# Kernel tuning notes

Hardware: AMD Instinct MI355X
Metric: run time of the kernel (lower is better)

The kernel has to match this reference:

```python
import jax, jax.numpy as jnp
import numpy as np

N, E = 100000, 3200000
F_IN, HID, NCLS = 1433, 8, 7
H1, H2 = 8, 1
NEG_SLOPE = 0.2


def gat_layer(x, W, att_src, att_dst, bias, src, dst, heads, ch):
    n = x.shape[0]
    h = (x @ W).reshape(n, heads, ch)                      # [N,H,C]
    a_s = (h * att_src).sum(-1)                            # [N,H]
    a_d = (h * att_dst).sum(-1)                            # [N,H]
    e = a_s[src] + a_d[dst]                                # [Etot,H]
    e = jnp.where(e > 0, e, NEG_SLOPE * e)                 # leaky_relu(0.2)
    m = jax.ops.segment_max(e, dst, num_segments=n)        # per-dst max
    e = jnp.exp(e - m[dst])
    denom = jax.ops.segment_sum(e, dst, num_segments=n)
    alpha = e / (denom[dst] + 1e-16)                       # segment softmax
    msg = h[src] * alpha[:, :, None]                       # [Etot,H,C]
    out = jax.ops.segment_sum(msg, dst, num_segments=n)    # [N,H,C]
    return out.mean(axis=1) + bias                         # concat=False -> head mean


def setup_inputs() -> dict:
    key = jax.random.key(0)
    ks = jax.random.split(key, 10)
    x = jax.random.normal(ks[0], (N, F_IN), dtype=jnp.float32)
    edge_index = jax.random.randint(ks[1], (2, E), 0, N, dtype=jnp.int32)
    s = 0.1
    W1 = jax.random.normal(ks[2], (F_IN, H1 * HID), dtype=jnp.float32) * s
    att_src1 = jax.random.normal(ks[3], (H1, HID), dtype=jnp.float32) * s
    att_dst1 = jax.random.normal(ks[4], (H1, HID), dtype=jnp.float32) * s
    b1 = jnp.zeros((HID,), dtype=jnp.float32)
    W2 = jax.random.normal(ks[5], (HID, H2 * NCLS), dtype=jnp.float32) * s
    att_src2 = jax.random.normal(ks[6], (H2, NCLS), dtype=jnp.float32) * s
    att_dst2 = jax.random.normal(ks[7], (H2, NCLS), dtype=jnp.float32) * s
    b2 = jnp.zeros((NCLS,), dtype=jnp.float32)
    return {"x": x, "edge_index": edge_index, "W1": W1, "att_src1": att_src1,
            "att_dst1": att_dst1, "b1": b1, "W2": W2, "att_src2": att_src2,
            "att_dst2": att_dst2, "b2": b2}


def reference(x, edge_index, W1, att_src1, att_dst1, b1, W2, att_src2, att_dst2, b2):
    n = x.shape[0]
    loops = jnp.arange(n, dtype=edge_index.dtype)
    src = jnp.concatenate([edge_index[0], loops])  # PyG add_self_loops=True
    dst = jnp.concatenate([edge_index[1], loops])
    h = jax.nn.elu(gat_layer(x, W1, att_src1, att_dst1, b1, src, dst, H1, HID))
    out = gat_layer(h, W2, att_src2, att_dst2, b2, src, dst, H2, NCLS)
    return jax.nn.log_softmax(out, axis=-1)
```

## Files before the change

### kernel.cpp

```cpp
#include <hip/hip_runtime.h>

#define N_NODES 100000
#define E_EDGES 3200000
#define F_IN    1433
#define K_PAD   1472
#define NCH     98
#define KPH     64

typedef _Float16 f16x4 __attribute__((ext_vector_type(4)));
typedef _Float16 f16x8 __attribute__((ext_vector_type(8)));
typedef float    f32x4 __attribute__((ext_vector_type(4)));

__device__ __forceinline__ void gload_lds16(const void* g, void* l) {
    __builtin_amdgcn_global_load_lds(
        (const __attribute__((address_space(1))) unsigned int*)g,
        (__attribute__((address_space(3))) unsigned int*)l, 16, 0, 0);
}

__global__ void k_init(const float* __restrict__ w1, _Float16* __restrict__ w1t,
                       int* __restrict__ counts) {
    int i = blockIdx.x * 256 + threadIdx.x;
    if (i < N_NODES) counts[i] = 0;
    if (i < 64 * K_PAD) {
        int n = i / K_PAD, k = i - n * K_PAD;
        float v = (k < F_IN) ? w1[(size_t)k * 64 + n] : 0.f;
        w1t[i] = (_Float16)v;
    }
}

__global__ void k_hist(const int* __restrict__ dst, int* __restrict__ counts) {
    int idx = blockIdx.x * 256 + threadIdx.x;
    int4 d4 = ((const int4*)dst)[idx];
    atomicAdd(&counts[d4.x], 1);
    atomicAdd(&counts[d4.y], 1);
    atomicAdd(&counts[d4.z], 1);
    atomicAdd(&counts[d4.w], 1);
}

__global__ void k_scan_a(const int* __restrict__ counts, int* __restrict__ csum) {
    __shared__ int sh[256];
    int b = blockIdx.x, t = threadIdx.x;
    int s = 0;
    for (int j = 0; j < 4; ++j) {
        int idx = b * 1024 + j * 256 + t;
        if (idx < N_NODES) s += counts[idx];
    }
    sh[t] = s; __syncthreads();
    for (int off = 128; off > 0; off >>= 1) {
        if (t < off) sh[t] += sh[t + off];
        __syncthreads();
    }
    if (t == 0) csum[b] = sh[0];
}

__global__ void k_scan_b(int* __restrict__ csum) {
    __shared__ int sh[128];
    int t = threadIdx.x;
    int v = (t < NCH) ? csum[t] : 0;
    sh[t] = v; __syncthreads();
    for (int off = 1; off < 128; off <<= 1) {
        int u = (t >= off) ? sh[t - off] : 0;
        __syncthreads();
        sh[t] += u;
        __syncthreads();
    }
    if (t < NCH) csum[t] = sh[t] - v;
}

__global__ void k_scan_c(const int* __restrict__ counts, const int* __restrict__ csum,
                         int* __restrict__ offsets, int* __restrict__ cursor) {
    __shared__ int sh[256];
    int b = blockIdx.x, t = threadIdx.x;
    int base = b * 1024 + t * 4;
    int c0 = (base + 0 < N_NODES) ? counts[base + 0] : 0;
    int c1 = (base + 1 < N_NODES) ? counts[base + 1] : 0;
    int c2 = (base + 2 < N_NODES) ? counts[base + 2] : 0;
    int c3 = (base + 3 < N_NODES) ? counts[base + 3] : 0;
    int tot = c0 + c1 + c2 + c3;
    sh[t] = tot; __syncthreads();
    for (int off = 1; off < 256; off <<= 1) {
        int v = (t >= off) ? sh[t - off] : 0;
        __syncthreads();
        sh[t] += v;
        __syncthreads();
    }
    int excl = sh[t] - tot;
    int o = csum[b] + excl;
    if (base + 0 < N_NODES) { offsets[base + 0] = o;            cursor[base + 0] = o; }
    if (base + 1 < N_NODES) { int q = o + c0;      offsets[base + 1] = q; cursor[base + 1] = q; }
    if (base + 2 < N_NODES) { int q = o + c0 + c1; offsets[base + 2] = q; cursor[base + 2] = q; }
    if (base + 3 < N_NODES) { int q = o + c0 + c1 + c2; offsets[base + 3] = q; cursor[base + 3] = q; }
}

__global__ __launch_bounds__(256) void k_gemm_scat(const float* __restrict__ x,
                                                   const _Float16* __restrict__ w1t,
                                                   const float* __restrict__ att_src1,
                                                   const float* __restrict__ att_dst1,
                                                   _Float16* __restrict__ h1,
                                                   float* __restrict__ a_s1,
                                                   float* __restrict__ a_d1,
                                                   const int* __restrict__ src,
                                                   const int* __restrict__ dst,
                                                   int* __restrict__ cursor,
                                                   int* __restrict__ sorted_src) {
    __shared__ __align__(16) char AsB[2][64 * 256];
    __shared__ __align__(16) char BsB[2][64 * 128];
    const int tid = threadIdx.x;

    if (blockIdx.x & 1) {
        const int sid = blockIdx.x >> 1;
        for (int sweep = 0; sweep < 7; ++sweep) {
            #pragma unroll
            for (int rep = 0; rep < 2; ++rep) {
                int i4 = sid * 512 + rep * 256 + tid;
                if (i4 < E_EDGES / 4) {
                    int4 s4 = ((const int4*)src)[i4];
                    int4 d4 = ((const int4*)dst)[i4];
                    int p;
                    if ((d4.x >> 14) == sweep) { p = atomicAdd(&cursor[d4.x], 1); sorted_src[p] = s4.x; }
                    if ((d4.y >> 14) == sweep) { p = atomicAdd(&cursor[d4.y], 1); sorted_src[p] = s4.y; }
                    if ((d4.z >> 14) == sweep) { p = atomicAdd(&cursor[d4.z], 1); sorted_src[p] = s4.z; }
                    if ((d4.w >> 14) == sweep) { p = atomicAdd(&cursor[d4.w], 1); sorted_src[p] = s4.w; }
                }
            }
        }
        return;
    }

    const int gid  = blockIdx.x >> 1;
    const int lane = tid & 63;
    const int wave = tid >> 6;
    const int l16  = lane & 15;
    const int l4   = lane >> 4;
    const int brow0 = gid * 64;

    f32x4 acc[4] = {};

    auto stageA = [&](int buf, int ph) {
        #pragma unroll
        for (int j = 0; j < 4; ++j) {
            int p = j * 256 + tid;
            int row = p >> 4, q = p & 15;
            int qs = q ^ (row & 7);
            int grow = brow0 + row; if (grow > N_NODES - 1) grow = N_NODES - 1;
            const float* gp = x + (size_t)grow * F_IN + ph * KPH + qs * 4;
            gload_lds16(gp, AsB[buf] + j * 4096 + wave * 1024);
        }
    };
    auto stageB = [&](int buf, int ph) {
        #pragma unroll
        for (int j = 0; j < 2; ++j) {
            int p = j * 256 + tid;
            int col = p >> 3, c = p & 7;
            int cs = c ^ (col & 7);
            const _Float16* gp = w1t + (size_t)col * K_PAD + ph * KPH + cs * 8;
            gload_lds16(gp, BsB[buf] + j * 4096 + wave * 1024);
        }
    };
    auto stageTailA = [&](int buf) {
        for (int i = tid; i < 1024; i += 256) {
            int row = i >> 4, q = i & 15;
            int qs = q ^ (row & 7);
            int grow = brow0 + row; if (grow > N_NODES - 1) grow = N_NODES - 1;
            const float* gp = x + (size_t)grow * F_IN;
            float4 v;
            #pragma unroll
            for (int jj = 0; jj < 4; ++jj) {
                int k = 1408 + qs * 4 + jj;
                ((float*)&v)[jj] = (k < F_IN) ? gp[k] : 0.f;
            }
            *(float4*)(AsB[buf] + row * 256 + q * 16) = v;
        }
    };
    auto compute = [&](int buf) {
        const int rA = wave * 16 + l16;
        const char* Ab = AsB[buf] + rA * 256;
        const int r7 = rA & 7;
        #pragma unroll
        for (int st = 0; st < 4; ++st) {
            float4 af = *(const float4*)(Ab + ((((st << 2) + l4) ^ r7) << 4));
            f16x4 a = { (_Float16)af.x, (_Float16)af.y, (_Float16)af.z, (_Float16)af.w };
            #pragma unroll
            for (int t = 0; t < 4; ++t) {
                const int cB = t * 16 + l16;
                const int chunk = (st << 1) + (l4 >> 1);
                const int boff = cB * 128 + ((chunk ^ (cB & 7)) << 4) + ((l4 & 1) << 3);
                f16x4 b = *(const f16x4*)(BsB[buf] + boff);
                acc[t] = __builtin_amdgcn_mfma_f32_16x16x16f16(a, b, acc[t], 0, 0, 0);
            }
        }
    };

    stageA(0, 0); stageB(0, 0);
    stageA(1, 1); stageB(1, 1);
    for (int ph = 0; ph <= 20; ++ph) {
        asm volatile("s_waitcnt vmcnt(6)" ::: "memory");
        __builtin_amdgcn_sched_barrier(0);
        __builtin_amdgcn_s_barrier();
        compute(ph & 1);
        asm volatile("s_waitcnt lgkmcnt(0)" ::: "memory");
        __builtin_amdgcn_s_barrier();
        int nxt = ph + 2;
        if (nxt < 22)       { stageA(ph & 1, nxt); stageB(ph & 1, nxt); }
        else if (nxt == 22) { stageTailA(ph & 1);  stageB(ph & 1, 22);  }
    }
    asm volatile("s_waitcnt vmcnt(0) lgkmcnt(0)" ::: "memory");
    __builtin_amdgcn_sched_barrier(0);
    __builtin_amdgcn_s_barrier();
    compute(1);
    compute(0);

    const int wrow0 = brow0 + wave * 16;
    #pragma unroll
    for (int t = 0; t < 4; ++t) {
        const int head = t * 2 + (l16 >> 3);
        const int ch   = l16 & 7;
        const float asc = att_src1[head * 8 + ch];
        const float adc = att_dst1[head * 8 + ch];
        #pragma unroll
        for (int j = 0; j < 4; ++j) {
            int r = wrow0 + l4 * 4 + j;
            float ps = acc[t][j] * asc, pd = acc[t][j] * adc;
            ps += __shfl_xor(ps, 1); ps += __shfl_xor(ps, 2); ps += __shfl_xor(ps, 4);
            pd += __shfl_xor(pd, 1); pd += __shfl_xor(pd, 2); pd += __shfl_xor(pd, 4);
            if (r < N_NODES) {
                h1[(size_t)r * 64 + t * 16 + l16] = (_Float16)acc[t][j];
                if (ch == 0) {
                    a_s1[r * 8 + head] = ps;
                    a_d1[r * 8 + head] = pd;
                }
            }
        }
    }
}

__global__ __launch_bounds__(256) void k_agg1(
    const int* __restrict__ offsets, const int* __restrict__ counts,
    const int* __restrict__ sorted_src,
    const float* __restrict__ a_s1, const float* __restrict__ a_d1,
    const _Float16* __restrict__ h1, const float* __restrict__ b1,
    const float* __restrict__ w2, const float* __restrict__ att_src2,
    const float* __restrict__ att_dst2,
    _Float16* __restrict__ g, float* __restrict__ a_s2, float* __restrict__ a_d2) {
    const int lane = threadIdx.x & 63;
    const int wave = threadIdx.x >> 6;
    const int h    = lane & 7;
    const int es   = lane >> 3;
    const int n    = blockIdx.x * 4 + wave;
    const int start = offsets[n];
    const int cnt   = counts[n];
    const float adn = a_d1[n * 8 + h];
    float et = a_s1[n * 8 + h] + adn;
    const float e_self = et > 0.f ? et : 0.2f * et;

    float m = e_self, denom = 0.f;
    float acc[8] = {0.f,0.f,0.f,0.f,0.f,0.f,0.f,0.f};
    if (es == 0) {
        denom = 1.f;
        f16x8 hv0 = *(const f16x8*)(h1 + (size_t)n * 64 + h * 8);
        #pragma unroll
        for (int c = 0; c < 8; ++c) acc[c] = (float)hv0[c];
    }
    for (int i = es; i < cnt; i += 64) {
        int   sx[8];
        float ax[8];
        f16x8 vx[8];
        bool  bx[8];
        #pragma unroll
        for (int u = 0; u < 8; ++u) {
            int iu = i + u * 8;
            bx[u] = iu < cnt;
            sx[u] = sorted_src[start + (bx[u] ? iu : i)];
        }
        #pragma unroll
        for (int u = 0; u < 8; ++u) ax[u] = a_s1[sx[u] * 8 + h];
        #pragma unroll
        for (int u = 0; u < 8; ++u) vx[u] = *(const f16x8*)(h1 + (size_t)sx[u] * 64 + h * 8);
        #pragma unroll
        for (int u = 0; u < 8; ++u) {
            if (bx[u]) {
                float e = ax[u] + adn; e = e > 0.f ? e : 0.2f * e;
                if (e > m + 8.f) {
                    float sc = __expf(m - e); denom *= sc;
                    #pragma unroll
                    for (int c = 0; c < 8; ++c) acc[c] *= sc;
                    m = e;
                }
                float p = __expf(e - m); denom += p;
                #pragma unroll
                for (int c = 0; c < 8; ++c) acc[c] += p * (float)vx[u][c];
            }
        }
    }
    #pragma unroll
    for (int d = 8; d < 64; d <<= 1) {
        float mo = __shfl_xor(m, d);
        float dn = __shfl_xor(denom, d);
        float mn = fmaxf(m, mo);
        float sa = __expf(m - mn), sb = __expf(mo - mn);
        denom = denom * sa + dn * sb;
        #pragma unroll
        for (int c = 0; c < 8; ++c) {
            float ao = __shfl_xor(acc[c], d);
            acc[c] = acc[c] * sa + ao * sb;
        }
        m = mn;
    }
    float inv = 1.f / (denom + 1e-16f);
    float hc[8];
    #pragma unroll
    for (int c = 0; c < 8; ++c) {
        float v = acc[c] * inv;
        v += __shfl_xor(v, 1);
        v += __shfl_xor(v, 2);
        v += __shfl_xor(v, 4);
        float o = 0.125f * v + b1[c];
        hc[c] = o > 0.f ? o : expm1f(o);
    }
    if (lane == 0) {
        float s2 = 0.f, d2 = 0.f;
        f16x8 gr;
        #pragma unroll
        for (int j = 0; j < 7; ++j) {
            float t = 0.f;
            #pragma unroll
            for (int c = 0; c < 8; ++c) t += hc[c] * w2[c * 7 + j];
            gr[j] = (_Float16)t;
            s2 += t * att_src2[j];
            d2 += t * att_dst2[j];
        }
        gr[7] = (_Float16)0.f;
        *(f16x8*)(g + (size_t)n * 8) = gr;
        a_s2[n] = s2;
        a_d2[n] = d2;
    }
}

__global__ __launch_bounds__(256) void k_agg2(
    const int* __restrict__ offsets, const int* __restrict__ counts,
    const int* __restrict__ sorted_src,
    const float* __restrict__ a_s2, const float* __restrict__ a_d2,
    const _Float16* __restrict__ g, const float* __restrict__ b2,
    float* __restrict__ outp) {
    const int tid  = threadIdx.x;
    const int lane = tid & 63;
    const int wave = tid >> 6;
    const int grp  = lane >> 3;
    const int s    = lane & 7;
    const int n    = blockIdx.x * 32 + wave * 8 + grp;
    const int start = offsets[n];
    const int cnt   = counts[n];
    const float adn = a_d2[n];
    float et = a_s2[n] + adn;
    const float e_self = et > 0.f ? et : 0.2f * et;

    float m = e_self, denom = 0.f;
    float acc[8] = {0.f,0.f,0.f,0.f,0.f,0.f,0.f,0.f};
    if (s == 0) {
        denom = 1.f;
        f16x8 gv0 = *(const f16x8*)(g + (size_t)n * 8);
        #pragma unroll
        for (int c = 0; c < 8; ++c) acc[c] = (float)gv0[c];
    }
    for (int i = s; i < cnt; i += 64) {
        int   sx[8];
        float ax[8];
        f16x8 vx[8];
        bool  bx[8];
        #pragma unroll
        for (int u = 0; u < 8; ++u) {
            int iu = i + u * 8;
            bx[u] = iu < cnt;
            sx[u] = sorted_src[start + (bx[u] ? iu : i)];
        }
        #pragma unroll
        for (int u = 0; u < 8; ++u) ax[u] = a_s2[sx[u]];
        #pragma unroll
        for (int u = 0; u < 8; ++u) vx[u] = *(const f16x8*)(g + (size_t)sx[u] * 8);
        #pragma unroll
        for (int u = 0; u < 8; ++u) {
            if (bx[u]) {
                float e = ax[u] + adn; e = e > 0.f ? e : 0.2f * e;
                if (e > m + 8.f) {
                    float sc = __expf(m - e); denom *= sc;
                    #pragma unroll
                    for (int c = 0; c < 8; ++c) acc[c] *= sc;
                    m = e;
                }
                float p = __expf(e - m); denom += p;
                #pragma unroll
                for (int c = 0; c < 8; ++c) acc[c] += p * (float)vx[u][c];
            }
        }
    }
    #pragma unroll
    for (int d = 1; d < 8; d <<= 1) {
        float mo = __shfl_xor(m, d, 8);
        float dn = __shfl_xor(denom, d, 8);
        float mn = fmaxf(m, mo);
        float sa = __expf(m - mn), sb = __expf(mo - mn);
        denom = denom * sa + dn * sb;
        #pragma unroll
        for (int c = 0; c < 8; ++c) {
            float ao = __shfl_xor(acc[c], d, 8);
            acc[c] = acc[c] * sa + ao * sb;
        }
        m = mn;
    }
    float inv = 1.f / (denom + 1e-16f);
    float o[7]; float mx = -1e30f;
    #pragma unroll
    for (int c = 0; c < 7; ++c) { o[c] = acc[c] * inv + b2[c]; mx = fmaxf(mx, o[c]); }
    float se = 0.f;
    #pragma unroll
    for (int c = 0; c < 7; ++c) se += __expf(o[c] - mx);
    float ls = mx + logf(se);
    if (s < 7) outp[n * 7 + s] = o[s] - ls;
}

extern "C" void kernel_launch(void* const* d_in, const int* in_sizes, int n_in,
                              void* d_out, int out_size, void* d_ws, size_t ws_size,
                              hipStream_t stream) {
    const float* x        = (const float*)d_in[0];
    const int*   ei       = (const int*)d_in[1];
    const float* W1       = (const float*)d_in[2];
    const float* att_src1 = (const float*)d_in[3];
    const float* att_dst1 = (const float*)d_in[4];
    const float* b1       = (const float*)d_in[5];
    const float* W2       = (const float*)d_in[6];
    const float* att_src2 = (const float*)d_in[7];
    const float* att_dst2 = (const float*)d_in[8];
    const float* b2       = (const float*)d_in[9];
    const int* src = ei;
    const int* dst = ei + E_EDGES;

    char* ws = (char*)d_ws;
    size_t off = 0;
    auto alloc = [&](size_t bytes) -> char* {
        char* p = ws + off;
        off = (off + bytes + 255) & ~(size_t)255;
        return p;
    };
    _Float16* h1         = (_Float16*)alloc((size_t)N_NODES * 64 * 2);
    float*    a_s1       = (float*)   alloc((size_t)N_NODES * 8 * 4);
    float*    a_d1       = (float*)   alloc((size_t)N_NODES * 8 * 4);
    _Float16* w1t        = (_Float16*)alloc((size_t)64 * K_PAD * 2);
    int*      counts     = (int*)     alloc((size_t)N_NODES * 4);
    int*      offsets    = (int*)     alloc((size_t)N_NODES * 4);
    int*      cursor     = (int*)     alloc((size_t)N_NODES * 4);
    int*      csum       = (int*)     alloc((size_t)NCH * 4);
    int*      sorted_src = (int*)     alloc((size_t)(E_EDGES + 32) * 4);
    _Float16* gbuf       = (_Float16*)alloc((size_t)N_NODES * 8 * 2);
    float*    a_s2       = (float*)   alloc((size_t)N_NODES * 4);
    float*    a_d2       = (float*)   alloc((size_t)N_NODES * 4);
    float*    outp       = (float*)d_out;

    hipLaunchKernelGGL(k_init,      dim3(391),   dim3(256), 0, stream, W1, w1t, counts);
    hipLaunchKernelGGL(k_hist,      dim3(3125),  dim3(256), 0, stream, dst, counts);
    hipLaunchKernelGGL(k_scan_a,    dim3(NCH),   dim3(256), 0, stream, counts, csum);
    hipLaunchKernelGGL(k_scan_b,    dim3(1),     dim3(128), 0, stream, csum);
    hipLaunchKernelGGL(k_scan_c,    dim3(NCH),   dim3(256), 0, stream, counts, csum, offsets, cursor);
    hipLaunchKernelGGL(k_gemm_scat, dim3(3126),  dim3(256), 0, stream,
                       x, w1t, att_src1, att_dst1, h1, a_s1, a_d1,
                       src, dst, cursor, sorted_src);
    hipLaunchKernelGGL(k_agg1,      dim3(25000), dim3(256), 0, stream, offsets, counts, sorted_src,
                       a_s1, a_d1, h1, b1, W2, att_src2, att_dst2, gbuf, a_s2, a_d2);
    hipLaunchKernelGGL(k_agg2,      dim3(3125),  dim3(256), 0, stream, offsets, counts, sorted_src,
                       a_s2, a_d2, gbuf, b2, outp);
}
```

Measured before the change: 538.6 us.

## Split scatter from GEMM and use single-wave 32-row GEMM blocks without barriers

The edge scatter, previously interleaved with GEMM blocks in one kernel, becomes its own kernel. The first-layer GEMM is rewritten as 64-thread single-wavefront blocks, each covering 32 rows with two row tiles, so the workgroup s_barriers disappear and each block reuses its B tile across more rows. Tail handling is restructured and the row clamp is dropped because 100000 divides evenly by 32. This gives up concurrent overlap of the atomic scatter with the GEMM and adds a kernel launch. In return it aims for less sync and better per-wave B reuse.

```diff
diff --git a/kernel.cpp b/kernel.cpp
--- a/kernel.cpp
+++ b/kernel.cpp
@@ -92,77 +92,70 @@
     if (base + 3 < N_NODES) { int q = o + c0 + c1 + c2; offsets[base + 3] = q; cursor[base + 3] = q; }
 }
 
-__global__ __launch_bounds__(256) void k_gemm_scat(const float* __restrict__ x,
-                                                   const _Float16* __restrict__ w1t,
-                                                   const float* __restrict__ att_src1,
-                                                   const float* __restrict__ att_dst1,
-                                                   _Float16* __restrict__ h1,
-                                                   float* __restrict__ a_s1,
-                                                   float* __restrict__ a_d1,
-                                                   const int* __restrict__ src,
-                                                   const int* __restrict__ dst,
-                                                   int* __restrict__ cursor,
-                                                   int* __restrict__ sorted_src) {
-    __shared__ __align__(16) char AsB[2][64 * 256];
+__global__ void k_scatter(const int* __restrict__ src, const int* __restrict__ dst,
+                          int* __restrict__ cursor, int* __restrict__ sorted_src) {
+    const int tid = threadIdx.x;
+    const int sid = blockIdx.x;
+    for (int sweep = 0; sweep < 7; ++sweep) {
+        #pragma unroll
+        for (int rep = 0; rep < 2; ++rep) {
+            int i4 = sid * 512 + rep * 256 + tid;
+            if (i4 < E_EDGES / 4) {
+                int4 s4 = ((const int4*)src)[i4];
+                int4 d4 = ((const int4*)dst)[i4];
+                int p;
+                if ((d4.x >> 14) == sweep) { p = atomicAdd(&cursor[d4.x], 1); sorted_src[p] = s4.x; }
+                if ((d4.y >> 14) == sweep) { p = atomicAdd(&cursor[d4.y], 1); sorted_src[p] = s4.y; }
+                if ((d4.z >> 14) == sweep) { p = atomicAdd(&cursor[d4.z], 1); sorted_src[p] = s4.z; }
+                if ((d4.w >> 14) == sweep) { p = atomicAdd(&cursor[d4.w], 1); sorted_src[p] = s4.w; }
+            }
+        }
+    }
+}
+
+__global__ __launch_bounds__(64) void k_gemm1(const float* __restrict__ x,
+                                              const _Float16* __restrict__ w1t,
+                                              const float* __restrict__ att_src1,
+                                              const float* __restrict__ att_dst1,
+                                              _Float16* __restrict__ h1,
+                                              float* __restrict__ a_s1,
+                                              float* __restrict__ a_d1) {
+    __shared__ __align__(16) char AsB[2][32 * 256];
     __shared__ __align__(16) char BsB[2][64 * 128];
-    const int tid = threadIdx.x;
-
-    if (blockIdx.x & 1) {
-        const int sid = blockIdx.x >> 1;
-        for (int sweep = 0; sweep < 7; ++sweep) {
-            #pragma unroll
-            for (int rep = 0; rep < 2; ++rep) {
-                int i4 = sid * 512 + rep * 256 + tid;
-                if (i4 < E_EDGES / 4) {
-                    int4 s4 = ((const int4*)src)[i4];
-                    int4 d4 = ((const int4*)dst)[i4];
-                    int p;
-                    if ((d4.x >> 14) == sweep) { p = atomicAdd(&cursor[d4.x], 1); sorted_src[p] = s4.x; }
-                    if ((d4.y >> 14) == sweep) { p = atomicAdd(&cursor[d4.y], 1); sorted_src[p] = s4.y; }
-                    if ((d4.z >> 14) == sweep) { p = atomicAdd(&cursor[d4.z], 1); sorted_src[p] = s4.z; }
-                    if ((d4.w >> 14) == sweep) { p = atomicAdd(&cursor[d4.w], 1); sorted_src[p] = s4.w; }
-                }
-            }
-        }
-        return;
-    }
-
-    const int gid  = blockIdx.x >> 1;
-    const int lane = tid & 63;
-    const int wave = tid >> 6;
+    const int lane = threadIdx.x & 63;
     const int l16  = lane & 15;
     const int l4   = lane >> 4;
-    const int brow0 = gid * 64;
-
-    f32x4 acc[4] = {};
+    const int brow0 = blockIdx.x * 32;
+
+    f32x4 acc[2][4] = {};
 
     auto stageA = [&](int buf, int ph) {
         #pragma unroll
-        for (int j = 0; j < 4; ++j) {
-            int p = j * 256 + tid;
+        for (int j = 0; j < 8; ++j) {
+            int p = j * 64 + lane;
             int row = p >> 4, q = p & 15;
             int qs = q ^ (row & 7);
-            int grow = brow0 + row; if (grow > N_NODES - 1) grow = N_NODES - 1;
-            const float* gp = x + (size_t)grow * F_IN + ph * KPH + qs * 4;
-            gload_lds16(gp, AsB[buf] + j * 4096 + wave * 1024);
+            const float* gp = x + (size_t)(brow0 + row) * F_IN + ph * KPH + qs * 4;
+            gload_lds16(gp, AsB[buf] + j * 1024);
         }
     };
     auto stageB = [&](int buf, int ph) {
         #pragma unroll
-        for (int j = 0; j < 2; ++j) {
-            int p = j * 256 + tid;
+        for (int j = 0; j < 8; ++j) {
+            int p = j * 64 + lane;
             int col = p >> 3, c = p & 7;
             int cs = c ^ (col & 7);
             const _Float16* gp = w1t + (size_t)col * K_PAD + ph * KPH + cs * 8;
-            gload_lds16(gp, BsB[buf] + j * 4096 + wave * 1024);
+            gload_lds16(gp, BsB[buf] + j * 1024);
         }
     };
     auto stageTailA = [&](int buf) {
-        for (int i = tid; i < 1024; i += 256) {
-            int row = i >> 4, q = i & 15;
+        #pragma unroll
+        for (int j = 0; j < 8; ++j) {
+            int p = j * 64 + lane;
+            int row = p >> 4, q = p & 15;
             int qs = q ^ (row & 7);
-            int grow = brow0 + row; if (grow > N_NODES - 1) grow = N_NODES - 1;
-            const float* gp = x + (size_t)grow * F_IN;
+            const float* gp = x + (size_t)(brow0 + row) * F_IN;
             float4 v;
             #pragma unroll
             for (int jj = 0; jj < 4; ++jj) {
@@ -173,58 +166,66 @@
         }
     };
     auto compute = [&](int buf) {
-        const int rA = wave * 16 + l16;
-        const char* Ab = AsB[buf] + rA * 256;
-        const int r7 = rA & 7;
         #pragma unroll
         for (int st = 0; st < 4; ++st) {
-            float4 af = *(const float4*)(Ab + ((((st << 2) + l4) ^ r7) << 4));
-            f16x4 a = { (_Float16)af.x, (_Float16)af.y, (_Float16)af.z, (_Float16)af.w };
             #pragma unroll
-            for (int t = 0; t < 4; ++t) {
-                const int cB = t * 16 + l16;
-                const int chunk = (st << 1) + (l4 >> 1);
-                const int boff = cB * 128 + ((chunk ^ (cB & 7)) << 4) + ((l4 & 1) << 3);
-                f16x4 b = *(const f16x4*)(BsB[buf] + boff);
-                acc[t] = __builtin_amdgcn_mfma_f32_16x16x16f16(a, b, acc[t], 0, 0, 0);
+            for (int rt = 0; rt < 2; ++rt) {
+                const int rA = rt * 16 + l16;
+                float4 af = *(const float4*)(AsB[buf] + rA * 256
+                                             + ((((st << 2) + l4) ^ (rA & 7)) << 4));
+                f16x4 a = { (_Float16)af.x, (_Float16)af.y, (_Float16)af.z, (_Float16)af.w };
+                #pragma unroll
+                for (int t = 0; t < 4; ++t) {
+                    const int cB = t * 16 + l16;
+                    const int chunk = (st << 1) + (l4 >> 1);
+                    const int boff = cB * 128 + ((chunk ^ (cB & 7)) << 4) + ((l4 & 1) << 3);
+                    f16x4 b = *(const f16x4*)(BsB[buf] + boff);
+                    acc[rt][t] = __builtin_amdgcn_mfma_f32_16x16x16f16(a, b, acc[rt][t], 0, 0, 0);
+                }
             }
         }
     };
 
     stageA(0, 0); stageB(0, 0);
     stageA(1, 1); stageB(1, 1);
-    for (int ph = 0; ph <= 20; ++ph) {
-        asm volatile("s_waitcnt vmcnt(6)" ::: "memory");
+    for (int ph = 0; ph <= 19; ++ph) {
+        asm volatile("s_waitcnt vmcnt(16)" ::: "memory");
         __builtin_amdgcn_sched_barrier(0);
-        __builtin_amdgcn_s_barrier();
         compute(ph & 1);
         asm volatile("s_waitcnt lgkmcnt(0)" ::: "memory");
-        __builtin_amdgcn_s_barrier();
-        int nxt = ph + 2;
-        if (nxt < 22)       { stageA(ph & 1, nxt); stageB(ph & 1, nxt); }
-        else if (nxt == 22) { stageTailA(ph & 1);  stageB(ph & 1, 22);  }
-    }
+        __builtin_amdgcn_sched_barrier(0);
+        stageA(ph & 1, ph + 2); stageB(ph & 1, ph + 2);
+    }
+    asm volatile("s_waitcnt vmcnt(16)" ::: "memory");
+    __builtin_amdgcn_sched_barrier(0);
+    compute(0);
+    asm volatile("s_waitcnt lgkmcnt(0)" ::: "memory");
+    __builtin_amdgcn_sched_barrier(0);
+    stageB(0, 22);
+    stageTailA(0);
+    asm volatile("s_waitcnt vmcnt(8)" ::: "memory");
+    __builtin_amdgcn_sched_barrier(0);
+    compute(1);
     asm volatile("s_waitcnt vmcnt(0) lgkmcnt(0)" ::: "memory");
     __builtin_amdgcn_sched_barrier(0);
-    __builtin_amdgcn_s_barrier();
-    compute(1);
     compute(0);
 
-    const int wrow0 = brow0 + wave * 16;
-    #pragma unroll
-    for (int t = 0; t < 4; ++t) {
-        const int head = t * 2 + (l16 >> 3);
-        const int ch   = l16 & 7;
-        const float asc = att_src1[head * 8 + ch];
-        const float adc = att_dst1[head * 8 + ch];
-        #pragma unroll
-        for (int j = 0; j < 4; ++j) {
-            int r = wrow0 + l4 * 4 + j;
-            float ps = acc[t][j] * asc, pd = acc[t][j] * adc;
-            ps += __shfl_xor(ps, 1); ps += __shfl_xor(ps, 2); ps += __shfl_xor(ps, 4);
-            pd += __shfl_xor(pd, 1); pd += __shfl_xor(pd, 2); pd += __shfl_xor(pd, 4);
-            if (r < N_NODES) {
-                h1[(size_t)r * 64 + t * 16 + l16] = (_Float16)acc[t][j];
+    #pragma unroll
+    for (int rt = 0; rt < 2; ++rt) {
+        const int wrow0 = brow0 + rt * 16;
+        #pragma unroll
+        for (int t = 0; t < 4; ++t) {
+            const int head = t * 2 + (l16 >> 3);
+            const int ch   = l16 & 7;
+            const float asc = att_src1[head * 8 + ch];
+            const float adc = att_dst1[head * 8 + ch];
+            #pragma unroll
+            for (int j = 0; j < 4; ++j) {
+                int r = wrow0 + l4 * 4 + j;
+                float ps = acc[rt][t][j] * asc, pd = acc[rt][t][j] * adc;
+                ps += __shfl_xor(ps, 1); ps += __shfl_xor(ps, 2); ps += __shfl_xor(ps, 4);
+                pd += __shfl_xor(pd, 1); pd += __shfl_xor(pd, 2); pd += __shfl_xor(pd, 4);
+                h1[(size_t)r * 64 + t * 16 + l16] = (_Float16)acc[rt][t][j];
                 if (ch == 0) {
                     a_s1[r * 8 + head] = ps;
                     a_d1[r * 8 + head] = pd;
@@ -455,16 +456,16 @@
     float*    a_d2       = (float*)   alloc((size_t)N_NODES * 4);
     float*    outp       = (float*)d_out;
 
-    hipLaunchKernelGGL(k_init,      dim3(391),   dim3(256), 0, stream, W1, w1t, counts);
-    hipLaunchKernelGGL(k_hist,      dim3(3125),  dim3(256), 0, stream, dst, counts);
-    hipLaunchKernelGGL(k_scan_a,    dim3(NCH),   dim3(256), 0, stream, counts, csum);
-    hipLaunchKernelGGL(k_scan_b,    dim3(1),     dim3(128), 0, stream, csum);
-    hipLaunchKernelGGL(k_scan_c,    dim3(NCH),   dim3(256), 0, stream, counts, csum, offsets, cursor);
-    hipLaunchKernelGGL(k_gemm_scat, dim3(3126),  dim3(256), 0, stream,
-                       x, w1t, att_src1, att_dst1, h1, a_s1, a_d1,
-                       src, dst, cursor, sorted_src);
-    hipLaunchKernelGGL(k_agg1,      dim3(25000), dim3(256), 0, stream, offsets, counts, sorted_src,
+    hipLaunchKernelGGL(k_init,    dim3(391),   dim3(256), 0, stream, W1, w1t, counts);
+    hipLaunchKernelGGL(k_hist,    dim3(3125),  dim3(256), 0, stream, dst, counts);
+    hipLaunchKernelGGL(k_scan_a,  dim3(NCH),   dim3(256), 0, stream, counts, csum);
+    hipLaunchKernelGGL(k_scan_b,  dim3(1),     dim3(128), 0, stream, csum);
+    hipLaunchKernelGGL(k_scan_c,  dim3(NCH),   dim3(256), 0, stream, counts, csum, offsets, cursor);
+    hipLaunchKernelGGL(k_scatter, dim3(1563),  dim3(256), 0, stream, src, dst, cursor, sorted_src);
+    hipLaunchKernelGGL(k_gemm1,   dim3(3125),  dim3(64),  0, stream, x, w1t, att_src1, att_dst1,
+                       h1, a_s1, a_d1);
+    hipLaunchKernelGGL(k_agg1,    dim3(25000), dim3(256), 0, stream, offsets, counts, sorted_src,
                        a_s1, a_d1, h1, b1, W2, att_src2, att_dst2, gbuf, a_s2, a_d2);
-    hipLaunchKernelGGL(k_agg2,      dim3(3125),  dim3(256), 0, stream, offsets, counts, sorted_src,
+    hipLaunchKernelGGL(k_agg2,    dim3(3125),  dim3(256), 0, stream, offsets, counts, sorted_src,
                        a_s2, a_d2, gbuf, b2, outp);
 }
```

New measurement: 622.9 us. 1.16x slower.
